# Kernel tuning notes

Hardware: AMD Instinct MI355X
Metric: run time of the kernel (lower is better)

The kernel has to match this reference:

```python
import jax, jax.numpy as jnp
import numpy as np

B, M, IN, H, D = 64, 512, 256, 4, 64
N = B * M
E = N * 16


def setup_inputs() -> dict:
    key = jax.random.key(0)
    ks = jax.random.split(key, 12)
    s = 1.0 / np.sqrt(IN)
    return {
        "query_input": jax.random.normal(ks[0], (N, IN), jnp.float32),
        "source_input": jax.random.normal(ks[1], (N, IN), jnp.float32),
        "edge_weight": jax.random.uniform(ks[2], (E,), jnp.float32),
        "Wq_w": jax.random.normal(ks[3], (IN, H * D), jnp.float32) * s,
        "Wq_b": jax.random.normal(ks[4], (H * D,), jnp.float32) * s,
        "Wk_w": jax.random.normal(ks[5], (IN, H * D), jnp.float32) * s,
        "Wk_b": jax.random.normal(ks[6], (H * D,), jnp.float32) * s,
        "Wv_w": jax.random.normal(ks[7], (IN, H * D), jnp.float32) * s,
        "Wv_b": jax.random.normal(ks[8], (H * D,), jnp.float32) * s,
        "n_nodes": jnp.full((B,), M, jnp.int32),
        "edge_index": jax.random.randint(ks[9], (2, E), 0, N, jnp.int32),
    }


def reference(query_input, source_input, edge_weight, Wq_w, Wq_b, Wk_w, Wk_b, Wv_w, Wv_b, n_nodes, edge_index):
    # projections -> [N, H, D]
    q = (query_input @ Wq_w + Wq_b).reshape(N, H, D)
    k = (source_input @ Wk_w + Wk_b).reshape(N, H, D)
    v = (source_input @ Wv_w + Wv_b).reshape(N, H, D)

    # 'simple' kernel attention. Global L2 normalization (torch.norm over whole tensor).
    qn = q / jnp.linalg.norm(q)
    kn = k / jnp.linalg.norm(k)
    # equal-size graphs: padding + mask reduces exactly to a reshape [B, M, H, D]
    q_pad = qn.reshape(B, M, H, D)
    k_pad = kn.reshape(B, M, H, D)
    v_pad = v.reshape(B, M, H, D)
    kv = jnp.einsum('bmhk,bmhv->bhkv', k_pad, v_pad)          # per-graph K^T V
    v_sum = v_pad.sum(axis=1)                                  # [B, H, D] scatter_add over batch
    k_sum = k_pad.sum(axis=1)                                  # [B, H, D]
    numer = jnp.einsum('bmhk,bhkv->bmhv', q_pad, kv) + v_sum[:, None]
    denom = jnp.einsum('bmhk,bhk->bmh', q_pad, k_sum) + n_nodes.astype(q.dtype)[:, None, None]
    attn = (numer / denom[..., None]).reshape(N, H, D)

    # gcn_conv on value: out[c] = sum_{e: col_e = c} w_e * rsqrt(deg[col_e]*deg[row_e]) * v[row_e]
    row, col = edge_index[0], edge_index[1]
    deg = jax.ops.segment_sum(jnp.ones((E,), jnp.float32), col, num_segments=N)
    val = edge_weight / jnp.sqrt(deg[col] * deg[row])
    val = jnp.nan_to_num(val, nan=0.0, posinf=0.0, neginf=0.0)
    gcn = jax.ops.segment_sum(val[:, None, None] * v[row], col, num_segments=N)

    return (attn + gcn).mean(axis=1)  # mean over heads -> [N, D]
```

## Files before the change

### kernel.cpp

```cpp
#include <hip/hip_runtime.h>
#include <hip/hip_bf16.h>

#define NN 32768
#define BB 64
#define MM 512
#define HH 4
#define DD 64
#define INF 256
#define HD 256
#define EE 524288
#define XSZ 8388608

typedef unsigned short ushort;
typedef unsigned int uint;
typedef short s16x8 __attribute__((ext_vector_type(8)));
typedef ushort u16x8 __attribute__((ext_vector_type(8)));
typedef float f32x4 __attribute__((ext_vector_type(4)));

__device__ __forceinline__ ushort f2bf(float f) {
    uint u = __float_as_uint(f);
    return (ushort)((u + 0x7fffu + ((u >> 16) & 1u)) >> 16);
}
__device__ __forceinline__ float bf2f(ushort u) {
    return __uint_as_float((uint)u << 16);
}
__device__ __forceinline__ uint pkbf(float x, float y) {
    __hip_bfloat162 h = __float22bfloat162_rn(make_float2(x, y));
    return *(uint*)&h;
}

#define GLD16(gp, lp) __builtin_amdgcn_global_load_lds( \
    (const __attribute__((address_space(1))) void*)(gp), \
    (__attribute__((address_space(3))) void*)(lp), 16, 0, 0)

__global__ __launch_bounds__(256) void prep_kernel(
    const float* __restrict__ Wq, const float* __restrict__ Wk,
    const float* __restrict__ Wv, ushort* __restrict__ WT,
    const int* __restrict__ ei, int* __restrict__ deg,
    const float* __restrict__ Xq, const float* __restrict__ Xs,
    ushort* __restrict__ xq16, ushort* __restrict__ xs16)
{
    const int bid = blockIdx.x;
    if (bid < 768) {
        const int id = bid * 256 + threadIdx.x;
        const int mat = id >> 16, rem = id & 65535;
        const int n = rem >> 8, kk = rem & 255;
        const float* W = (mat == 0) ? Wq : (mat == 1) ? Wk : Wv;
        WT[id] = f2bf(W[kk * 256 + n]);
    } else if (bid < 2816) {
        const int e = (bid - 768) * 256 + threadIdx.x;
        atomicAdd(&deg[ei[EE + e]], 1);
    } else {
        const size_t id = (size_t)(bid - 2816) * 256 + threadIdx.x;
        const size_t o8 = id * 8;
        const float* src; ushort* dst; size_t o;
        if (o8 < XSZ) { src = Xq; dst = xq16; o = o8; }
        else          { src = Xs; dst = xs16; o = o8 - XSZ; }
        const float4 f0 = *(const float4*)(src + o);
        const float4 f1 = *(const float4*)(src + o + 4);
        u16x8 r;
        r[0] = f2bf(f0.x); r[1] = f2bf(f0.y); r[2] = f2bf(f0.z); r[3] = f2bf(f0.w);
        r[4] = f2bf(f1.x); r[5] = f2bf(f1.y); r[6] = f2bf(f1.z); r[7] = f2bf(f1.w);
        *(u16x8*)(dst + o) = r;
    }
}

__global__ __launch_bounds__(256) void qkv_scan(
    const ushort* __restrict__ Xq16, const ushort* __restrict__ Xs16,
    const ushort* __restrict__ WT,
    const float* __restrict__ bq, const float* __restrict__ bk,
    const float* __restrict__ bv,
    ushort* __restrict__ qo, ushort* __restrict__ ko, ushort* __restrict__ vo,
    float* __restrict__ sumsq,
    const int* __restrict__ deg, int* __restrict__ offsets)
{
    __shared__ ushort As[3][128 * 32];
    __shared__ ushort Bs[3][128 * 32];
    __shared__ float wred[4];
    __shared__ int part[256];

    const int id = blockIdx.x;
    const int t = threadIdx.x;

    if (id == 1536) {
        const int base = t * 128;
        int s = 0;
        for (int i = 0; i < 128; ++i) s += deg[base + i];
        part[t] = s;
        __syncthreads();
        for (int off = 1; off < 256; off <<= 1) {
            int a = part[t];
            int b2 = (t >= off) ? part[t - off] : 0;
            __syncthreads();
            part[t] = a + b2;
            __syncthreads();
        }
        int run = (t == 0) ? 0 : part[t - 1];
        for (int i = 0; i < 128; ++i) { offsets[base + i] = run; run += deg[base + i]; }
        if (t == 255) offsets[NN] = run;
        return;
    }

    const int vv = (id & 7) * 192 + (id >> 3);
    const int rt = vv / 6, ct = vv % 6;
    const int wsel = ct >> 1;
    const ushort* A16 = (wsel == 0) ? Xq16 : Xs16;
    const ushort* W   = WT + (size_t)wsel * 65536;
    const float* bias = (wsel == 0) ? bq : (wsel == 1) ? bk : bv;
    ushort* C         = (wsel == 0) ? qo : (wsel == 1) ? ko : vo;
    const int row0 = rt * 128;
    const int col0 = (ct & 1) * 128;

    const int l = t & 63, w = t >> 6;
    const int fr = l & 15, q4 = l >> 4;
    const int wr = (w & 1) * 64, wc = (w >> 1) * 64;

    const int srow = (w << 4) + (l >> 2);
    const int scol = (l & 3) << 3;
    const ushort* ga = &A16[(size_t)(row0 + srow) * INF + scol];
    const ushort* gb = &W  [(size_t)(col0 + srow) * INF + scol];
    const int lbase = (w << 9);

    f32x4 acc[4][4] = {};

#define QKV_STAGE(bufi, k0) \
    GLD16(ga + (k0),            &As[bufi][lbase]); \
    GLD16(ga + (k0) + 64 * INF, &As[bufi][2048 + lbase]); \
    GLD16(gb + (k0),            &Bs[bufi][lbase]); \
    GLD16(gb + (k0) + 64 * INF, &Bs[bufi][2048 + lbase]);

#define QKV_COMPUTE(bufi) { \
    const int kg = q4 * 8; \
    s16x8 af[4], bfr[4]; \
    _Pragma("unroll") \
    for (int i = 0; i < 4; ++i) \
        af[i] = *(const s16x8*)&As[bufi][(wr + i * 16 + fr) * 32 + kg]; \
    _Pragma("unroll") \
    for (int j = 0; j < 4; ++j) \
        bfr[j] = *(const s16x8*)&Bs[bufi][(wc + j * 16 + fr) * 32 + kg]; \
    _Pragma("unroll") \
    for (int i = 0; i < 4; ++i) \
    _Pragma("unroll") \
        for (int j = 0; j < 4; ++j) \
            acc[i][j] = __builtin_amdgcn_mfma_f32_16x16x32_bf16( \
                af[i], bfr[j], acc[i][j], 0, 0, 0); }

#define WAIT4 asm volatile("s_waitcnt vmcnt(4)" ::: "memory")
#define WAIT0 asm volatile("s_waitcnt vmcnt(0)" ::: "memory")
#define BAR   __builtin_amdgcn_s_barrier()

    QKV_STAGE(0, 0)
    QKV_STAGE(1, 32)

    WAIT4; BAR; QKV_STAGE(2,  64) QKV_COMPUTE(0)
    WAIT4; BAR; QKV_STAGE(0,  96) QKV_COMPUTE(1)
    WAIT4; BAR; QKV_STAGE(1, 128) QKV_COMPUTE(2)
    WAIT4; BAR; QKV_STAGE(2, 160) QKV_COMPUTE(0)
    WAIT4; BAR; QKV_STAGE(0, 192) QKV_COMPUTE(1)
    WAIT4; BAR; QKV_STAGE(1, 224) QKV_COMPUTE(2)
    WAIT4; BAR;                   QKV_COMPUTE(0)
    WAIT0; BAR;                   QKV_COMPUTE(1)

    float loc = 0.f;
#pragma unroll
    for (int j = 0; j < 4; ++j) {
        const int colg = col0 + wc + j * 16 + fr;
        const float bj = bias[colg];
#pragma unroll
        for (int i = 0; i < 4; ++i) {
            const int rowg = row0 + wr + i * 16 + q4 * 4;
#pragma unroll
            for (int m = 0; m < 4; ++m) {
                float cv = acc[i][j][m] + bj;
                loc += cv * cv;
                C[(size_t)(rowg + m) * HD + colg] = f2bf(cv);
            }
        }
    }
    if (wsel < 2) {
#pragma unroll
        for (int off = 32; off > 0; off >>= 1) loc += __shfl_down(loc, off, 64);
        if (l == 0) wred[w] = loc;
        __syncthreads();
        if (t == 0) atomicAdd(&sumsq[wsel], wred[0] + wred[1] + wred[2] + wred[3]);
    }
}

#define KVP 136
__global__ __launch_bounds__(256) void kv_vbar(
    const ushort* __restrict__ k16, const ushort* __restrict__ v16,
    float* __restrict__ kv_p, float* __restrict__ ksum_p, float* __restrict__ vsum_p,
    float* __restrict__ vbar)
{
    __shared__ ushort kT[64 * KVP];
    __shared__ ushort vT[64 * KVP];
    const int bid = blockIdx.x;
    const int t = threadIdx.x;

    if (bid >= 1024) {
        const int idx = (bid - 1024) * 1024 + t * 4;
        const int n = idx >> 6, d0 = idx & 63;
        const ushort* vr = &v16[(size_t)n * HD + d0];
        float4 o;
        float* op = (float*)&o;
#pragma unroll
        for (int j = 0; j < 4; ++j)
            op[j] = 0.25f * (bf2f(vr[j]) + bf2f(vr[64 + j]) +
                             bf2f(vr[128 + j]) + bf2f(vr[192 + j]));
        *(float4*)&vbar[idx] = o;
        return;
    }

    const int h = bid & 3, b = (bid >> 2) & 63, z = bid >> 8;
    const int l = t & 63, w = t >> 6;
    const size_t base = (size_t)b * MM * HD + (size_t)h * DD;
    const int m0 = z * 128;

    {
        const int mat = t >> 7;
        const int u = t & 63;
        const int dhalf = (t >> 6) & 1;
        const int r0 = 2 * u;
        const int d0 = dhalf * 32;
        const ushort* src = mat ? v16 : k16;
        ushort* dst = mat ? vT : kT;
        const ushort* p0 = &src[base + (size_t)(m0 + r0) * HD + d0];
        const ushort* p1 = p0 + HD;
        u16x8 ra[4], rb[4];
#pragma unroll
        for (int i = 0; i < 4; ++i) ra[i] = *(const u16x8*)(p0 + 8 * i);
#pragma unroll
        for (int i = 0; i < 4; ++i) rb[i] = *(const u16x8*)(p1 + 8 * i);
#pragma unroll
        for (int i = 0; i < 4; ++i)
#pragma unroll
            for (int jj = 0; jj < 8; ++jj) {
                const int d = d0 + 8 * i + jj;
                uint pk = (uint)ra[i][jj] | ((uint)rb[i][jj] << 16);
                *(uint*)&dst[d * KVP + r0] = pk;
            }
    }
    __syncthreads();

    const int fr = l & 15, q4 = l >> 4, kg = q4 * 8;
    const int wr2 = (w & 1) * 32, wc2 = (w >> 1) * 32;
    s16x8 ones;
#pragma unroll
    for (int i = 0; i < 8; ++i) ones[i] = (short)0x3F80;

    f32x4 acc[2][2] = {};
    f32x4 aks[2] = {};
    f32x4 avs[2] = {};
#pragma unroll
    for (int s = 0; s < 4; ++s) {
        const int mo = s * 32 + kg;
        s16x8 af[2], bf[2];
        af[0] = *(const s16x8*)&kT[(wr2 + fr) * KVP + mo];
        af[1] = *(const s16x8*)&kT[(wr2 + 16 + fr) * KVP + mo];
        bf[0] = *(const s16x8*)&vT[(wc2 + fr) * KVP + mo];
        bf[1] = *(const s16x8*)&vT[(wc2 + 16 + fr) * KVP + mo];
#pragma unroll
        for (int il = 0; il < 2; ++il)
#pragma unroll
            for (int jl = 0; jl < 2; ++jl)
                acc[il][jl] = __builtin_amdgcn_mfma_f32_16x16x32_bf16(
                    af[il], bf[jl], acc[il][jl], 0, 0, 0);
#pragma unroll
        for (int il = 0; il < 2; ++il)
            aks[il] = __builtin_amdgcn_mfma_f32_16x16x32_bf16(
                af[il], ones, aks[il], 0, 0, 0);
#pragma unroll
        for (int jl = 0; jl < 2; ++jl)
            avs[jl] = __builtin_amdgcn_mfma_f32_16x16x32_bf16(
                ones, bf[jl], avs[jl], 0, 0, 0);
    }

    float* kvb = &kv_p[(((size_t)b * HH + h) * 4 + z) * 4096];
#pragma unroll
    for (int jl = 0; jl < 2; ++jl) {
        const int dv = wc2 + 16 * jl + fr;
#pragma unroll
        for (int il = 0; il < 2; ++il) {
            const int dk = wr2 + 16 * il + q4 * 4;
            *(f32x4*)&kvb[(size_t)dv * 64 + dk] = acc[il][jl];
        }
    }
    float* ksb = &ksum_p[(((size_t)b * HH + h) * 4 + z) * 64];
    float* vsb = &vsum_p[(((size_t)b * HH + h) * 4 + z) * 64];
    if (wc2 == 0 && fr == 0) {
#pragma unroll
        for (int il = 0; il < 2; ++il)
#pragma unroll
            for (int m = 0; m < 4; ++m)
                ksb[wr2 + 16 * il + q4 * 4 + m] = aks[il][m];
    }
    if (wr2 == 0 && l < 16) {
        vsb[wc2 + l]      = avs[0][0];
        vsb[wc2 + 16 + l] = avs[1][0];
    }
}

__global__ __launch_bounds__(256) void red_bucket(
    const float* __restrict__ kv_p, const float* __restrict__ ksum_p,
    const float* __restrict__ vsum_p,
    ushort* __restrict__ kv16, float* __restrict__ ksum_f, float* __restrict__ vsum_f,
    const int* __restrict__ ei, const float* __restrict__ ew,
    const int* __restrict__ deg, const int* __restrict__ offsets,
    int* __restrict__ cursor, int2* __restrict__ pairbuf)
{
    const int bid = blockIdx.x;
    const int t = threadIdx.x;

    if (bid < 1024) {
        const int o4 = bid * 1024 + t * 4;
        const int bh = o4 >> 12, off = o4 & 4095;
        const float* p = &kv_p[(size_t)bh * 16384 + off];
        float4 s0 = *(const float4*)p;
        float4 s1 = *(const float4*)(p + 4096);
        float4 s2 = *(const float4*)(p + 8192);
        float4 s3 = *(const float4*)(p + 12288);
        const float r0 = s0.x + s1.x + s2.x + s3.x;
        const float r1 = s0.y + s1.y + s2.y + s3.y;
        const float r2 = s0.z + s1.z + s2.z + s3.z;
        const float r3 = s0.w + s1.w + s2.w + s3.w;
        uint2 pk = make_uint2(pkbf(r0, r1), pkbf(r2, r3));
        *(uint2*)&kv16[(size_t)bh * 4096 + off] = pk;
    } else if (bid < 1152) {
        const int o = (bid - 1024) * 256 + t;
        const float* src = (o < 16384) ? ksum_p : vsum_p;
        float* dst = (o < 16384) ? ksum_f : vsum_f;
        const int oo = o & 16383;
        const int bh = oo >> 6, d = oo & 63;
        const float* p = &src[(size_t)bh * 256 + d];
        dst[oo] = p[0] + p[64] + p[128] + p[192];
    } else {
        const int e = (bid - 1152) * 256 + t;
        const int row = ei[e], col = ei[EE + e];
        const long long prod = (long long)deg[row] * (long long)deg[col];
        float val = 0.f;
        if (prod > 0) val = ew[e] * __frsqrt_rn((float)prod);
        const int pos = atomicAdd(&cursor[col], 1);
        pairbuf[offsets[col] + pos] = make_int2(row, __float_as_int(val));
    }
}

#define AKP 72
__global__ __launch_bounds__(256) void attn_mfma(
    const ushort* __restrict__ q16, const ushort* __restrict__ kv16,
    const float* __restrict__ ksum_f, const float* __restrict__ vsum_f,
    const float* __restrict__ sumsq,
    const int* __restrict__ n_nodes, float* __restrict__ out)
{
    const int b = blockIdx.y;
    const int m0 = blockIdx.x * 64;
    const int t = threadIdx.x;
    const int l = t & 63, w = t >> 6;
    const int fr = l & 15, q4 = l >> 4;
    const int wn = (w & 1) * 32, wd = (w >> 1) * 32;

    __shared__ ushort kvbf[HH][64 * AKP];
    __shared__ float ksum_l[HH][64], vsum_l[HH][64], denom_l[HH][64];

    const float nn = (float)n_nodes[b];
    const float inv = 1.0f / (sqrtf(sumsq[0]) * sqrtf(sumsq[1]));

    {
        const int dv = t >> 2, dk0 = (t & 3) * 16;
#pragma unroll
        for (int h = 0; h < HH; ++h) {
            const ushort* kvg = &kv16[((size_t)(b * HH + h)) * 4096 + dv * 64 + dk0];
            *(uint4*)&kvbf[h][dv * AKP + dk0]     = *(const uint4*)kvg;
            *(uint4*)&kvbf[h][dv * AKP + dk0 + 8] = *(const uint4*)(kvg + 8);
        }
        const int hh = t >> 6, dd = t & 63;
        ksum_l[hh][dd] = ksum_f[((size_t)(b * HH + hh)) * 64 + dd];
        vsum_l[hh][dd] = vsum_f[((size_t)(b * HH + hh)) * 64 + dd];
    }
    __syncthreads();

    {
        const int r = t & 63, hh = t >> 6;
        const ushort* qr = &q16[((size_t)(b * MM + m0 + r)) * HD + hh * DD];
        float dsum = 0.f;
#pragma unroll
        for (int c = 0; c < 8; ++c) {
            u16x8 qv = *(const u16x8*)(qr + 8 * c);
#pragma unroll
            for (int j2 = 0; j2 < 8; ++j2)
                dsum += bf2f(qv[j2]) * ksum_l[hh][8 * c + j2];
        }
        denom_l[hh][r] = nn + inv * dsum;
    }
    __syncthreads();

    f32x4 acco[2][2] = {};
#pragma unroll
    for (int h = 0; h < HH; ++h) {
        f32x4 pacc[2][2] = {};
#pragma unroll
        for (int kx = 0; kx < 2; ++kx) {
            const int k0 = kx * 32;
            s16x8 af[2], bfr[2];
#pragma unroll
            for (int il = 0; il < 2; ++il)
                af[il] = *(const s16x8*)&q16[
                    ((size_t)(b * MM + m0 + wn + 16 * il + fr)) * HD + h * DD + k0 + q4 * 8];
#pragma unroll
            for (int jl = 0; jl < 2; ++jl)
                bfr[jl] = *(const s16x8*)&kvbf[h][(wd + 16 * jl + fr) * AKP + k0 + q4 * 8];
#pragma unroll
            for (int il = 0; il < 2; ++il)
#pragma unroll
                for (int jl = 0; jl < 2; ++jl)
                    pacc[il][jl] = __builtin_amdgcn_mfma_f32_16x16x32_bf16(
                        af[il], bfr[jl], pacc[il][jl], 0, 0, 0);
        }
#pragma unroll
        for (int il = 0; il < 2; ++il)
#pragma unroll
            for (int m = 0; m < 4; ++m) {
                const float rden = 0.25f / denom_l[h][wn + 16 * il + q4 * 4 + m];
#pragma unroll
                for (int jl = 0; jl < 2; ++jl) {
                    const int d = wd + 16 * jl + fr;
                    acco[il][jl][m] += (inv * pacc[il][jl][m] + vsum_l[h][d]) * rden;
                }
            }
    }

#pragma unroll
    for (int il = 0; il < 2; ++il)
#pragma unroll
        for (int m = 0; m < 4; ++m) {
            const size_t node = (size_t)b * MM + m0 + wn + 16 * il + q4 * 4 + m;
#pragma unroll
            for (int jl = 0; jl < 2; ++jl)
                out[node * DD + wd + 16 * jl + fr] = acco[il][jl][m];
        }
}

__global__ __launch_bounds__(256) void gcn_gather(
    const int* __restrict__ offsets, const int2* __restrict__ pairbuf,
    const float* __restrict__ vbar, float* __restrict__ out)
{
    const int t = blockIdx.x * 256 + threadIdx.x;
    const int n = t >> 5;
    const int g = t & 31;
    const int d4 = (g & 15) << 2;
    const int grp = g >> 4;
    const int s = offsets[n], e = offsets[n + 1];
    float ax = 0.f, ay = 0.f, az = 0.f, aw = 0.f;
    int i = s + grp;
    for (; i + 2 < e; i += 4) {
        const int2 p0 = pairbuf[i], p1 = pairbuf[i + 2];
        const float w0 = __int_as_float(p0.y), w1 = __int_as_float(p1.y);
        const float4 v0 = *(const float4*)&vbar[(size_t)p0.x * DD + d4];
        const float4 v1 = *(const float4*)&vbar[(size_t)p1.x * DD + d4];
        ax += w0 * v0.x + w1 * v1.x;
        ay += w0 * v0.y + w1 * v1.y;
        az += w0 * v0.z + w1 * v1.z;
        aw += w0 * v0.w + w1 * v1.w;
    }
    if (i < e) {
        const int2 p = pairbuf[i];
        const float wv = __int_as_float(p.y);
        const float4 v = *(const float4*)&vbar[(size_t)p.x * DD + d4];
        ax += wv * v.x; ay += wv * v.y; az += wv * v.z; aw += wv * v.w;
    }
    ax += __shfl_xor(ax, 16, 64);
    ay += __shfl_xor(ay, 16, 64);
    az += __shfl_xor(az, 16, 64);
    aw += __shfl_xor(aw, 16, 64);
    if (grp == 0) {
        float4 o = *(float4*)&out[(size_t)n * DD + d4];
        o.x += ax; o.y += ay; o.z += az; o.w += aw;
        *(float4*)&out[(size_t)n * DD + d4] = o;
    }
}

extern "C" void kernel_launch(void* const* d_in, const int* in_sizes, int n_in,
                              void* d_out, int out_size, void* d_ws, size_t ws_size,
                              hipStream_t stream)
{
    (void)in_sizes; (void)n_in; (void)out_size; (void)ws_size;
    const float* Xq = (const float*)d_in[0];
    const float* Xs = (const float*)d_in[1];
    const float* ew = (const float*)d_in[2];
    const float* Wq = (const float*)d_in[3];
    const float* bq = (const float*)d_in[4];
    const float* Wk = (const float*)d_in[5];
    const float* bk = (const float*)d_in[6];
    const float* Wv = (const float*)d_in[7];
    const float* bv = (const float*)d_in[8];
    const int* n_nodes = (const int*)d_in[9];
    const int* ei = (const int*)d_in[10];
    float* out = (float*)d_out;
    float* ws  = (float*)d_ws;

    const size_t SZ_QKV   = (size_t)NN * HD / 2;
    const size_t OFF_Q    = 0;
    const size_t OFF_K    = SZ_QKV;
    const size_t OFF_V    = SZ_QKV * 2;
    const size_t OFF_SS   = SZ_QKV * 3;
    const size_t OFF_DEG  = OFF_SS + 16;
    const size_t OFF_CUR  = OFF_DEG + NN;
    const size_t OFF_WT   = OFF_CUR + NN;
    const size_t OFF_OFFS = OFF_WT + 3 * 65536 / 2;
    const size_t OFF_UNI  = OFF_OFFS + NN + 16;
    const size_t OFF_XQ16 = OFF_UNI;
    const size_t OFF_XS16 = OFF_UNI + XSZ / 2;
    const size_t OFF_KV   = OFF_UNI;
    const size_t OFF_KSP  = OFF_KV + (size_t)BB * HH * 4 * 4096;
    const size_t OFF_VSP  = OFF_KSP + (size_t)BB * HH * 4 * 64;
    const size_t OFF_KV16 = OFF_VSP + (size_t)BB * HH * 4 * 64;
    const size_t OFF_KSF  = OFF_KV16 + (size_t)BB * HH * 4096 / 2;
    const size_t OFF_VSF  = OFF_KSF + (size_t)BB * HH * 64;
    const size_t OFF_PAIR = OFF_VSF + (size_t)BB * HH * 64;
    const size_t OFF_VBAR = OFF_PAIR + 2 * (size_t)EE;

    ushort* q16   = (ushort*)(ws + OFF_Q);
    ushort* k16   = (ushort*)(ws + OFF_K);
    ushort* v16   = (ushort*)(ws + OFF_V);
    float* sumsq  = ws + OFF_SS;
    int*   deg    = (int*)(ws + OFF_DEG);
    int*   cursor = (int*)(ws + OFF_CUR);
    ushort* WT    = (ushort*)(ws + OFF_WT);
    int*   offs   = (int*)(ws + OFF_OFFS);
    ushort* xq16  = (ushort*)(ws + OFF_XQ16);
    ushort* xs16  = (ushort*)(ws + OFF_XS16);
    float* kv_p   = ws + OFF_KV;
    float* ksum_p = ws + OFF_KSP;
    float* vsum_p = ws + OFF_VSP;
    ushort* kv16  = (ushort*)(ws + OFF_KV16);
    float* ksum_f = ws + OFF_KSF;
    float* vsum_f = ws + OFF_VSF;
    int2*  pairb  = (int2*)(ws + OFF_PAIR);
    float* vbar   = ws + OFF_VBAR;

    hipMemsetAsync(sumsq, 0, (16 + 2 * NN) * sizeof(float), stream);
    prep_kernel<<<11008, 256, 0, stream>>>(Wq, Wk, Wv, WT, ei, deg, Xq, Xs, xq16, xs16);
    qkv_scan<<<1537, 256, 0, stream>>>(
        xq16, xs16, WT, bq, bk, bv, q16, k16, v16, sumsq, deg, offs);
    kv_vbar<<<3072, 256, 0, stream>>>(k16, v16, kv_p, ksum_p, vsum_p, vbar);
    red_bucket<<<3200, 256, 0, stream>>>(
        kv_p, ksum_p, vsum_p, kv16, ksum_f, vsum_f,
        ei, ew, deg, offs, cursor, pairb);
    attn_mfma<<<dim3(MM / 64, BB), 256, 0, stream>>>(
        q16, kv16, ksum_f, vsum_f, sumsq, n_nodes, out);
    gcn_gather<<<(NN * 32) / 256, 256, 0, stream>>>(offs, pairb, vbar, out);
}
```

Before: 255.5 us.

## Fuse KV partial reduction into kv kernel by looping over node chunks

Each (batch, head) block now loops over all four 128-row chunks and accumulates K^T V, k_sum and v_sum in registers instead of writing four fp32 partials and reducing them in a separate kernel. The edge bucketing work moves into the same launch, which removes one kernel launch and the partial-buffer round trip through memory. The trade-off is that only 256 blocks do the KV work, each running four times longer, so parallelism for that phase drops while the bucketing and vbar blocks fill the rest of the GPU.

```diff
diff --git a/kernel.cpp b/kernel.cpp
--- a/kernel.cpp
+++ b/kernel.cpp
@@ -187,160 +187,136 @@
 }
 
 #define KVP 136
-__global__ __launch_bounds__(256) void kv_vbar(
+__global__ __launch_bounds__(256) void kv_vbar_bucket(
     const ushort* __restrict__ k16, const ushort* __restrict__ v16,
-    float* __restrict__ kv_p, float* __restrict__ ksum_p, float* __restrict__ vsum_p,
-    float* __restrict__ vbar)
+    ushort* __restrict__ kv16, float* __restrict__ ksum_f, float* __restrict__ vsum_f,
+    float* __restrict__ vbar,
+    const int* __restrict__ ei, const float* __restrict__ ew,
+    const int* __restrict__ deg, const int* __restrict__ offsets,
+    int* __restrict__ cursor, int2* __restrict__ pairbuf)
 {
     __shared__ ushort kT[64 * KVP];
     __shared__ ushort vT[64 * KVP];
     const int bid = blockIdx.x;
     const int t = threadIdx.x;
 
-    if (bid >= 1024) {
-        const int idx = (bid - 1024) * 1024 + t * 4;
-        const int n = idx >> 6, d0 = idx & 63;
-        const ushort* vr = &v16[(size_t)n * HD + d0];
-        float4 o;
-        float* op = (float*)&o;
-#pragma unroll
-        for (int j = 0; j < 4; ++j)
-            op[j] = 0.25f * (bf2f(vr[j]) + bf2f(vr[64 + j]) +
-                             bf2f(vr[128 + j]) + bf2f(vr[192 + j]));
-        *(float4*)&vbar[idx] = o;
-        return;
-    }
-
-    const int h = bid & 3, b = (bid >> 2) & 63, z = bid >> 8;
-    const int l = t & 63, w = t >> 6;
-    const size_t base = (size_t)b * MM * HD + (size_t)h * DD;
-    const int m0 = z * 128;
-
-    {
-        const int mat = t >> 7;
-        const int u = t & 63;
-        const int dhalf = (t >> 6) & 1;
-        const int r0 = 2 * u;
-        const int d0 = dhalf * 32;
-        const ushort* src = mat ? v16 : k16;
-        ushort* dst = mat ? vT : kT;
-        const ushort* p0 = &src[base + (size_t)(m0 + r0) * HD + d0];
-        const ushort* p1 = p0 + HD;
-        u16x8 ra[4], rb[4];
-#pragma unroll
-        for (int i = 0; i < 4; ++i) ra[i] = *(const u16x8*)(p0 + 8 * i);
-#pragma unroll
-        for (int i = 0; i < 4; ++i) rb[i] = *(const u16x8*)(p1 + 8 * i);
-#pragma unroll
-        for (int i = 0; i < 4; ++i)
-#pragma unroll
-            for (int jj = 0; jj < 8; ++jj) {
-                const int d = d0 + 8 * i + jj;
-                uint pk = (uint)ra[i][jj] | ((uint)rb[i][jj] << 16);
-                *(uint*)&dst[d * KVP + r0] = pk;
-            }
-    }
-    __syncthreads();
-
-    const int fr = l & 15, q4 = l >> 4, kg = q4 * 8;
-    const int wr2 = (w & 1) * 32, wc2 = (w >> 1) * 32;
-    s16x8 ones;
-#pragma unroll
-    for (int i = 0; i < 8; ++i) ones[i] = (short)0x3F80;
-
-    f32x4 acc[2][2] = {};
-    f32x4 aks[2] = {};
-    f32x4 avs[2] = {};
-#pragma unroll
-    for (int s = 0; s < 4; ++s) {
-        const int mo = s * 32 + kg;
-        s16x8 af[2], bf[2];
-        af[0] = *(const s16x8*)&kT[(wr2 + fr) * KVP + mo];
-        af[1] = *(const s16x8*)&kT[(wr2 + 16 + fr) * KVP + mo];
-        bf[0] = *(const s16x8*)&vT[(wc2 + fr) * KVP + mo];
-        bf[1] = *(const s16x8*)&vT[(wc2 + 16 + fr) * KVP + mo];
-#pragma unroll
-        for (int il = 0; il < 2; ++il)
-#pragma unroll
-            for (int jl = 0; jl < 2; ++jl)
-                acc[il][jl] = __builtin_amdgcn_mfma_f32_16x16x32_bf16(
-                    af[il], bf[jl], acc[il][jl], 0, 0, 0);
-#pragma unroll
-        for (int il = 0; il < 2; ++il)
-            aks[il] = __builtin_amdgcn_mfma_f32_16x16x32_bf16(
-                af[il], ones, aks[il], 0, 0, 0);
-#pragma unroll
-        for (int jl = 0; jl < 2; ++jl)
-            avs[jl] = __builtin_amdgcn_mfma_f32_16x16x32_bf16(
-                ones, bf[jl], avs[jl], 0, 0, 0);
-    }
-
-    float* kvb = &kv_p[(((size_t)b * HH + h) * 4 + z) * 4096];
-#pragma unroll
-    for (int jl = 0; jl < 2; ++jl) {
-        const int dv = wc2 + 16 * jl + fr;
-#pragma unroll
-        for (int il = 0; il < 2; ++il) {
-            const int dk = wr2 + 16 * il + q4 * 4;
-            *(f32x4*)&kvb[(size_t)dv * 64 + dk] = acc[il][jl];
-        }
-    }
-    float* ksb = &ksum_p[(((size_t)b * HH + h) * 4 + z) * 64];
-    float* vsb = &vsum_p[(((size_t)b * HH + h) * 4 + z) * 64];
-    if (wc2 == 0 && fr == 0) {
-#pragma unroll
-        for (int il = 0; il < 2; ++il)
-#pragma unroll
-            for (int m = 0; m < 4; ++m)
-                ksb[wr2 + 16 * il + q4 * 4 + m] = aks[il][m];
-    }
-    if (wr2 == 0 && l < 16) {
-        vsb[wc2 + l]      = avs[0][0];
-        vsb[wc2 + 16 + l] = avs[1][0];
-    }
-}
-
-__global__ __launch_bounds__(256) void red_bucket(
-    const float* __restrict__ kv_p, const float* __restrict__ ksum_p,
-    const float* __restrict__ vsum_p,
-    ushort* __restrict__ kv16, float* __restrict__ ksum_f, float* __restrict__ vsum_f,
-    const int* __restrict__ ei, const float* __restrict__ ew,
-    const int* __restrict__ deg, const int* __restrict__ offsets,
-    int* __restrict__ cursor, int2* __restrict__ pairbuf)
-{
-    const int bid = blockIdx.x;
-    const int t = threadIdx.x;
-
-    if (bid < 1024) {
-        const int o4 = bid * 1024 + t * 4;
-        const int bh = o4 >> 12, off = o4 & 4095;
-        const float* p = &kv_p[(size_t)bh * 16384 + off];
-        float4 s0 = *(const float4*)p;
-        float4 s1 = *(const float4*)(p + 4096);
-        float4 s2 = *(const float4*)(p + 8192);
-        float4 s3 = *(const float4*)(p + 12288);
-        const float r0 = s0.x + s1.x + s2.x + s3.x;
-        const float r1 = s0.y + s1.y + s2.y + s3.y;
-        const float r2 = s0.z + s1.z + s2.z + s3.z;
-        const float r3 = s0.w + s1.w + s2.w + s3.w;
-        uint2 pk = make_uint2(pkbf(r0, r1), pkbf(r2, r3));
-        *(uint2*)&kv16[(size_t)bh * 4096 + off] = pk;
-    } else if (bid < 1152) {
-        const int o = (bid - 1024) * 256 + t;
-        const float* src = (o < 16384) ? ksum_p : vsum_p;
-        float* dst = (o < 16384) ? ksum_f : vsum_f;
-        const int oo = o & 16383;
-        const int bh = oo >> 6, d = oo & 63;
-        const float* p = &src[(size_t)bh * 256 + d];
-        dst[oo] = p[0] + p[64] + p[128] + p[192];
-    } else {
-        const int e = (bid - 1152) * 256 + t;
+    if (bid >= 2304) {
+        const int e = (bid - 2304) * 256 + t;
         const int row = ei[e], col = ei[EE + e];
         const long long prod = (long long)deg[row] * (long long)deg[col];
         float val = 0.f;
         if (prod > 0) val = ew[e] * __frsqrt_rn((float)prod);
         const int pos = atomicAdd(&cursor[col], 1);
         pairbuf[offsets[col] + pos] = make_int2(row, __float_as_int(val));
+        return;
+    }
+    if (bid >= 256) {
+        const int idx = (bid - 256) * 1024 + t * 4;
+        const int n = idx >> 6, d0 = idx & 63;
+        const ushort* vr = &v16[(size_t)n * HD + d0];
+        float4 o;
+        float* op = (float*)&o;
+#pragma unroll
+        for (int j = 0; j < 4; ++j)
+            op[j] = 0.25f * (bf2f(vr[j]) + bf2f(vr[64 + j]) +
+                             bf2f(vr[128 + j]) + bf2f(vr[192 + j]));
+        *(float4*)&vbar[idx] = o;
+        return;
+    }
+
+    const int h = bid & 3, b = bid >> 2;
+    const int l = t & 63, w = t >> 6;
+    const size_t base = (size_t)b * MM * HD + (size_t)h * DD;
+
+    const int fr = l & 15, q4 = l >> 4, kg = q4 * 8;
+    const int wr2 = (w & 1) * 32, wc2 = (w >> 1) * 32;
+    s16x8 ones;
+#pragma unroll
+    for (int i = 0; i < 8; ++i) ones[i] = (short)0x3F80;
+
+    f32x4 acc[2][2] = {};
+    f32x4 aks[2] = {};
+    f32x4 avs[2] = {};
+
+    const int mat = t >> 7;
+    const int u = t & 63;
+    const int dhalf = (t >> 6) & 1;
+    const int r0 = 2 * u;
+    const int d0 = dhalf * 32;
+    const ushort* src = mat ? v16 : k16;
+    ushort* dst = mat ? vT : kT;
+
+    for (int chunk = 0; chunk < 4; ++chunk) {
+        const int m0 = chunk * 128;
+        {
+            const ushort* p0 = &src[base + (size_t)(m0 + r0) * HD + d0];
+            const ushort* p1 = p0 + HD;
+            u16x8 ra[4], rb[4];
+#pragma unroll
+            for (int i = 0; i < 4; ++i) ra[i] = *(const u16x8*)(p0 + 8 * i);
+#pragma unroll
+            for (int i = 0; i < 4; ++i) rb[i] = *(const u16x8*)(p1 + 8 * i);
+#pragma unroll
+            for (int i = 0; i < 4; ++i)
+#pragma unroll
+                for (int jj = 0; jj < 8; ++jj) {
+                    const int d = d0 + 8 * i + jj;
+                    uint pk = (uint)ra[i][jj] | ((uint)rb[i][jj] << 16);
+                    *(uint*)&dst[d * KVP + r0] = pk;
+                }
+        }
+        __syncthreads();
+
+#pragma unroll
+        for (int s = 0; s < 4; ++s) {
+            const int mo = s * 32 + kg;
+            s16x8 af[2], bf[2];
+            af[0] = *(const s16x8*)&kT[(wr2 + fr) * KVP + mo];
+            af[1] = *(const s16x8*)&kT[(wr2 + 16 + fr) * KVP + mo];
+            bf[0] = *(const s16x8*)&vT[(wc2 + fr) * KVP + mo];
+            bf[1] = *(const s16x8*)&vT[(wc2 + 16 + fr) * KVP + mo];
+#pragma unroll
+            for (int il = 0; il < 2; ++il)
+#pragma unroll
+                for (int jl = 0; jl < 2; ++jl)
+                    acc[il][jl] = __builtin_amdgcn_mfma_f32_16x16x32_bf16(
+                        af[il], bf[jl], acc[il][jl], 0, 0, 0);
+#pragma unroll
+            for (int il = 0; il < 2; ++il)
+                aks[il] = __builtin_amdgcn_mfma_f32_16x16x32_bf16(
+                    af[il], ones, aks[il], 0, 0, 0);
+#pragma unroll
+            for (int jl = 0; jl < 2; ++jl)
+                avs[jl] = __builtin_amdgcn_mfma_f32_16x16x32_bf16(
+                    ones, bf[jl], avs[jl], 0, 0, 0);
+        }
+        __syncthreads();
+    }
+
+    ushort* kvb = &kv16[((size_t)b * HH + h) * 4096];
+#pragma unroll
+    for (int jl = 0; jl < 2; ++jl) {
+        const int dv = wc2 + 16 * jl + fr;
+#pragma unroll
+        for (int il = 0; il < 2; ++il) {
+            const int dk = wr2 + 16 * il + q4 * 4;
+            uint2 pk = make_uint2(pkbf(acc[il][jl][0], acc[il][jl][1]),
+                                  pkbf(acc[il][jl][2], acc[il][jl][3]));
+            *(uint2*)&kvb[(size_t)dv * 64 + dk] = pk;
+        }
+    }
+    float* ksb = &ksum_f[((size_t)b * HH + h) * 64];
+    float* vsb = &vsum_f[((size_t)b * HH + h) * 64];
+    if (wc2 == 0 && fr == 0) {
+#pragma unroll
+        for (int il = 0; il < 2; ++il)
+#pragma unroll
+            for (int m = 0; m < 4; ++m)
+                ksb[wr2 + 16 * il + q4 * 4 + m] = aks[il][m];
+    }
+    if (wr2 == 0 && l < 16) {
+        vsb[wc2 + l]      = avs[0][0];
+        vsb[wc2 + 16 + l] = avs[1][0];
     }
 }
 
@@ -509,10 +485,7 @@
     const size_t OFF_UNI  = OFF_OFFS + NN + 16;
     const size_t OFF_XQ16 = OFF_UNI;
     const size_t OFF_XS16 = OFF_UNI + XSZ / 2;
-    const size_t OFF_KV   = OFF_UNI;
-    const size_t OFF_KSP  = OFF_KV + (size_t)BB * HH * 4 * 4096;
-    const size_t OFF_VSP  = OFF_KSP + (size_t)BB * HH * 4 * 64;
-    const size_t OFF_KV16 = OFF_VSP + (size_t)BB * HH * 4 * 64;
+    const size_t OFF_KV16 = OFF_UNI;
     const size_t OFF_KSF  = OFF_KV16 + (size_t)BB * HH * 4096 / 2;
     const size_t OFF_VSF  = OFF_KSF + (size_t)BB * HH * 64;
     const size_t OFF_PAIR = OFF_VSF + (size_t)BB * HH * 64;
@@ -528,9 +501,6 @@
     int*   offs   = (int*)(ws + OFF_OFFS);
     ushort* xq16  = (ushort*)(ws + OFF_XQ16);
     ushort* xs16  = (ushort*)(ws + OFF_XS16);
-    float* kv_p   = ws + OFF_KV;
-    float* ksum_p = ws + OFF_KSP;
-    float* vsum_p = ws + OFF_VSP;
     ushort* kv16  = (ushort*)(ws + OFF_KV16);
     float* ksum_f = ws + OFF_KSF;
     float* vsum_f = ws + OFF_VSF;
@@ -541,10 +511,8 @@
     prep_kernel<<<11008, 256, 0, stream>>>(Wq, Wk, Wv, WT, ei, deg, Xq, Xs, xq16, xs16);
     qkv_scan<<<1537, 256, 0, stream>>>(
         xq16, xs16, WT, bq, bk, bv, q16, k16, v16, sumsq, deg, offs);
-    kv_vbar<<<3072, 256, 0, stream>>>(k16, v16, kv_p, ksum_p, vsum_p, vbar);
-    red_bucket<<<3200, 256, 0, stream>>>(
-        kv_p, ksum_p, vsum_p, kv16, ksum_f, vsum_f,
-        ei, ew, deg, offs, cursor, pairb);
+    kv_vbar_bucket<<<4352, 256, 0, stream>>>(
+        k16, v16, kv16, ksum_f, vsum_f, vbar, ei, ew, deg, offs, cursor, pairb);
     attn_mfma<<<dim3(MM / 64, BB), 256, 0, stream>>>(
         q16, kv16, ksum_f, vsum_f, sumsq, n_nodes, out);
     gcn_gather<<<(NN * 32) / 256, 256, 0, stream>>>(offs, pairb, vbar, out);
```

New measurement: 250.3 us. 1.02x faster.
